# Kernel tuning notes

Hardware: AMD Instinct MI355X
Metric: run time of the kernel (lower is better)

Reference implementation:

```python
import jax, jax.numpy as jnp
from jax import lax
import numpy as np

SEQ = 1024
VOCAB = 50000
EMB = 300
CAS_V, CAS_D = 8, 50
POS_V, POS_D = 48, 50
IN_DIM = EMB + CAS_D + POS_D  # 400
H = 512
T = 13  # num_classes / CRF tags


def setup_inputs() -> dict:
    key = jax.random.key(0)
    ks = jax.random.split(key, 16)
    s = lambda k, shape, sc=0.05: jax.random.normal(k, shape, dtype=jnp.float32) * sc
    return {
        "x": jax.random.randint(ks[0], (SEQ,), 0, VOCAB),
        "casing": jax.random.randint(ks[1], (SEQ,), 0, CAS_V),
        "pos": jax.random.randint(ks[2], (SEQ,), 0, POS_V),
        "h0": jnp.zeros((2, H), dtype=jnp.float32),
        "c0": jnp.zeros((2, H), dtype=jnp.float32),
        "W_emb": s(ks[3], (VOCAB, EMB)),
        "W_cas": s(ks[4], (CAS_V, CAS_D)),
        "W_pos": s(ks[5], (POS_V, POS_D)),
        "Wx_f": s(ks[6], (IN_DIM, 4 * H)),
        "Wh_f": s(ks[7], (H, 4 * H)),
        "b_f": jnp.zeros((4 * H,), dtype=jnp.float32),
        "Wx_b": s(ks[8], (IN_DIM, 4 * H)),
        "Wh_b": s(ks[9], (H, 4 * H)),
        "b_b": jnp.zeros((4 * H,), dtype=jnp.float32),
        "W_out": s(ks[10], (2 * H, T)),
        "b_out": jnp.zeros((T,), dtype=jnp.float32),
        "trans": s(ks[11], (T, T), 0.1),
        "start_trans": s(ks[12], (T,), 0.1),
        "end_trans": s(ks[13], (T,), 0.1),
    }


def _lstm_dir(feat, Wx, Wh, b, h0, c0, reverse):
    # feat: [L, IN_DIM]; precompute input projection for all steps
    pre = feat @ Wx + b  # [L, 4H]

    def step(carry, p):
        h, c = carry
        z = p + h @ Wh
        i, f, g, o = jnp.split(z, 4, axis=-1)
        c = jax.nn.sigmoid(f) * c + jax.nn.sigmoid(i) * jnp.tanh(g)
        h = jax.nn.sigmoid(o) * jnp.tanh(c)
        return (h, c), h

    _, hs = lax.scan(step, (h0, c0), pre, reverse=reverse)
    return hs  # [L, H]


def _viterbi(em, trans, start_trans, end_trans):
    # em: [L, T] emission (log) scores; max-plus DP
    score0 = start_trans + em[0]

    def fwd(score, e):
        total = score[:, None] + trans  # [T, T]: prev -> next
        best = jnp.max(total, axis=0) + e
        idx = jnp.argmax(total, axis=0)
        return best, idx

    final, hist = lax.scan(fwd, score0, em[1:])  # hist: [L-1, T]
    final = final + end_trans
    last = jnp.argmax(final)

    def back(tag, idx_row):
        return idx_row[tag], tag

    first, rest = lax.scan(back, last, hist, reverse=True)
    return jnp.concatenate([first[None], rest])  # [L] int


def reference(x, casing, pos, h0, c0, W_emb, W_cas, W_pos, Wx_f, Wh_f, b_f,
              Wx_b, Wh_b, b_b, W_out, b_out, trans, start_trans, end_trans):
    # AWD-LSTM encode (eval mode: dropout identity)
    feat = jnp.concatenate([W_emb[x], W_cas[casing], W_pos[pos]], axis=-1)  # [L, 400]
    hf = _lstm_dir(feat, Wx_f, Wh_f, b_f, h0[0], c0[0], reverse=False)
    hb = _lstm_dir(feat, Wx_b, Wh_b, b_b, h0[1], c0[1], reverse=True)
    o = jnp.concatenate([hf, hb], axis=-1) @ W_out + b_out  # [L, T]
    tag_scores = jax.nn.log_softmax(o, axis=1)
    path = _viterbi(tag_scores, trans, start_trans, end_trans)
    return tag_scores, path
```

## Files before the change

kernel.cpp:

```cpp
#include <hip/hip_runtime.h>
#include <hip/hip_bf16.h>
#include <math.h>

#define SEQ 1024
#define HID 512
#define FOURH 2048
#define IND 400
#define NT 13

#define NWG_DIR 32
#define LSTM_THREADS 512
#define JPW 16
#define WCOLS 64
#define TAG_INVALID 0xFFFFFFFFu

__device__ __forceinline__ float bf2f(unsigned short u) {
    union { unsigned u32; float f; } v;
    v.u32 = ((unsigned)u) << 16;
    return v.f;
}

__device__ __forceinline__ unsigned short f2bf(float f) {
    union { float f; unsigned u; } v;
    v.f = f;
    unsigned u = v.u;
    unsigned rounding = 0x7FFFu + ((u >> 16) & 1u);
    u += rounding;
    return (unsigned short)(u >> 16);
}

__device__ __forceinline__ float ldf(const void* p, size_t i, int isf32) {
    return isf32 ? ((const float*)p)[i] : bf2f(((const unsigned short*)p)[i]);
}

__device__ __forceinline__ float fsigm(float x) {
    return __builtin_amdgcn_rcpf(1.f + __builtin_amdgcn_exp2f(-1.44269504f * x));
}
__device__ __forceinline__ float ftanhf(float x) {
    return 1.f - 2.f * __builtin_amdgcn_rcpf(__builtin_amdgcn_exp2f(2.88539008f * x) + 1.f);
}
__device__ __forceinline__ float satz(float z) { return fminf(fmaxf(z, -60.f), 60.f); }

__global__ __launch_bounds__(64) void detect_kernel(const unsigned short* __restrict__ w,
                                                    int* __restrict__ flag,
                                                    unsigned* __restrict__ vcnt) {
    int lane = threadIdx.x;
    int cnt = 0;
    for (int i = 0; i < 4; ++i) {
        unsigned short u = w[2 * (lane * 4 + i)];
        int e = (u >> 7) & 0xFF;
        if (e >= 90 && e < 127) cnt++;
    }
#pragma unroll
    for (int off = 32; off >= 1; off >>= 1) cnt += __shfl_xor(cnt, off, 64);
    if (lane == 0) *flag = (cnt < 128) ? 1 : 0;
    if (lane == 1) *vcnt = 0;
}

__global__ __launch_bounds__(256) void pre_gemm_kernel(
        const int* __restrict__ x, const int* __restrict__ cas, const int* __restrict__ pos,
        const void* __restrict__ W_emb, const void* __restrict__ W_cas, const void* __restrict__ W_pos,
        const void* __restrict__ Wx_f, const void* __restrict__ b_f,
        const void* __restrict__ Wx_b, const void* __restrict__ b_b,
        unsigned short* __restrict__ pre, const int* __restrict__ dflag) {
    __shared__ float ftile[32 * IND];
    __shared__ int idxs[96];
    const int isf32 = *dflag;
    int dir = blockIdx.z;
    const void* Wx = dir ? Wx_b : Wx_f;
    const void* bb = dir ? b_b : b_f;
    unsigned short* pre_d = pre + (size_t)dir * SEQ * FOURH;
    int r0 = blockIdx.y * 32;
    int col = blockIdx.x * 256 + threadIdx.x;
    int tid = threadIdx.x;

    if (tid < 32)       idxs[tid] = x[r0 + tid];
    else if (tid < 64)  idxs[tid] = cas[r0 + tid - 32];
    else if (tid < 96)  idxs[tid] = pos[r0 + tid - 64];
    __syncthreads();

    for (int idx = tid; idx < 32 * IND; idx += 256) {
        int r = idx / IND;
        int e = idx - r * IND;
        float v;
        if (e < 300)      v = ldf(W_emb, (size_t)idxs[r] * 300 + e, isf32);
        else if (e < 350) v = ldf(W_cas, (size_t)idxs[32 + r] * 50 + (e - 300), isf32);
        else              v = ldf(W_pos, (size_t)idxs[64 + r] * 50 + (e - 350), isf32);
        ftile[idx] = v;
    }
    __syncthreads();

    float acc[32];
    float bias = ldf(bb, col, isf32);
#pragma unroll
    for (int r = 0; r < 32; ++r) acc[r] = bias;

    if (isf32) {
        const float* W = (const float*)Wx;
        for (int kk = 0; kk < 100; ++kk) {
            int k = kk * 4;
            float w0 = W[(size_t)(k + 0) * FOURH + col];
            float w1 = W[(size_t)(k + 1) * FOURH + col];
            float w2 = W[(size_t)(k + 2) * FOURH + col];
            float w3 = W[(size_t)(k + 3) * FOURH + col];
#pragma unroll
            for (int r = 0; r < 32; ++r) {
                float4 f = *(const float4*)&ftile[r * IND + k];
                acc[r] += f.x * w0 + f.y * w1 + f.z * w2 + f.w * w3;
            }
        }
    } else {
        const unsigned short* W = (const unsigned short*)Wx;
        for (int kk = 0; kk < 100; ++kk) {
            int k = kk * 4;
            float w0 = bf2f(W[(size_t)(k + 0) * FOURH + col]);
            float w1 = bf2f(W[(size_t)(k + 1) * FOURH + col]);
            float w2 = bf2f(W[(size_t)(k + 2) * FOURH + col]);
            float w3 = bf2f(W[(size_t)(k + 3) * FOURH + col]);
#pragma unroll
            for (int r = 0; r < 32; ++r) {
                float4 f = *(const float4*)&ftile[r * IND + k];
                acc[r] += f.x * w0 + f.y * w1 + f.z * w2 + f.w * w3;
            }
        }
    }
    for (int r = 0; r < 32; ++r) pre_d[(size_t)(r0 + r) * FOURH + col] = f2bf(acc[r]);
}

__global__ __launch_bounds__(LSTM_THREADS, 2) void lstm_kernel(
        const void* __restrict__ Wh_f, const void* __restrict__ Wh_b,
        const void* __restrict__ h0, const void* __restrict__ c0,
        const unsigned short* __restrict__ pre, float* __restrict__ hsout,
        unsigned long long* hbuf, const int* __restrict__ dflag) {
    __shared__ float hs[HID];
    __shared__ float red[8 * WCOLS];

    const int isf32 = *dflag;
    const int tid = threadIdx.x;
    const int b = blockIdx.x;
    const int dir = b & 1;
    const int g = b >> 1;
    const int j0 = g * JPW;

    const void* Wh = dir ? Wh_b : Wh_f;
    const unsigned short* pre_d = pre + (size_t)dir * SEQ * FOURH;
    float* hso = hsout + (size_t)dir * SEQ * HID;
    unsigned long long* hb_d = hbuf + dir * 2 * HID;

    const int seg  = tid >> 6;
    const int col  = tid & 63;
    const int unit = col & 15;
    const int gate = col >> 4;
    const int gcol = gate * HID + j0 + unit;
    const int redoff = seg * WCOLS + unit * 4 + gate;

    float wreg[64];
    if (isf32) {
        const float* wp = (const float*)Wh + (size_t)(seg * 64) * FOURH + gcol;
#pragma unroll
        for (int kk = 0; kk < 64; ++kk) wreg[kk] = wp[(size_t)kk * FOURH];
    } else {
        const unsigned short* wp = (const unsigned short*)Wh + (size_t)(seg * 64) * FOURH + gcol;
#pragma unroll
        for (int kk = 0; kk < 64; ++kk) wreg[kk] = bf2f(wp[(size_t)kk * FOURH]);
    }

    float creg = 0.f;
    unsigned short zn0 = 0, zn1 = 0, zn2 = 0, zn3 = 0;
    if (tid < JPW) {
        creg = ldf(c0, dir * HID + j0 + tid, isf32);
        float h0v = ldf(h0, dir * HID + j0 + tid, isf32);
        __hip_atomic_store(&hb_d[j0 + tid],
                           (unsigned long long)__float_as_uint(h0v),
                           __ATOMIC_RELAXED, __HIP_MEMORY_SCOPE_AGENT);
        __hip_atomic_store(&hb_d[HID + j0 + tid],
                           ((unsigned long long)TAG_INVALID << 32),
                           __ATOMIC_RELAXED, __HIP_MEMORY_SCOPE_AGENT);
        int t0 = dir ? (SEQ - 1) : 0;
        zn0 = pre_d[(size_t)t0 * FOURH + 0 * HID + j0 + tid];
        zn1 = pre_d[(size_t)t0 * FOURH + 1 * HID + j0 + tid];
        zn2 = pre_d[(size_t)t0 * FOURH + 2 * HID + j0 + tid];
        zn3 = pre_d[(size_t)t0 * FOURH + 3 * HID + j0 + tid];
    }
    __syncthreads();

    for (int s = 0; s < SEQ; ++s) {
        const int t = dir ? (SEQ - 1 - s) : s;

        {
            const unsigned long long* wp = &hb_d[(s & 1) * HID + tid];
            const unsigned expect = (unsigned)s;
            unsigned long long w;
            do {
                w = __hip_atomic_load(wp, __ATOMIC_RELAXED, __HIP_MEMORY_SCOPE_AGENT);
            } while ((unsigned)(w >> 32) != expect);
            hs[tid] = __uint_as_float((unsigned)w);
        }

        float zc0 = 0.f, zc1 = 0.f, zc2 = 0.f, zc3 = 0.f;
        if (tid < JPW) {
            zc0 = bf2f(zn0); zc1 = bf2f(zn1); zc2 = bf2f(zn2); zc3 = bf2f(zn3);
            if (s + 1 < SEQ) {
                int tn = dir ? (SEQ - 2 - s) : (s + 1);
                zn0 = pre_d[(size_t)tn * FOURH + 0 * HID + j0 + tid];
                zn1 = pre_d[(size_t)tn * FOURH + 1 * HID + j0 + tid];
                zn2 = pre_d[(size_t)tn * FOURH + 2 * HID + j0 + tid];
                zn3 = pre_d[(size_t)tn * FOURH + 3 * HID + j0 + tid];
            }
        }
        __syncthreads();

        float a0 = 0.f, a1 = 0.f, a2 = 0.f, a3 = 0.f;
        const float4* hp = (const float4*)(hs + seg * 64);
#pragma unroll
        for (int q = 0; q < 16; ++q) {
            float4 h4 = hp[q];
            int base = q * 4;
            if ((q & 3) == 0) a0 += h4.x * wreg[base] + h4.y * wreg[base + 1] + h4.z * wreg[base + 2] + h4.w * wreg[base + 3];
            if ((q & 3) == 1) a1 += h4.x * wreg[base] + h4.y * wreg[base + 1] + h4.z * wreg[base + 2] + h4.w * wreg[base + 3];
            if ((q & 3) == 2) a2 += h4.x * wreg[base] + h4.y * wreg[base + 1] + h4.z * wreg[base + 2] + h4.w * wreg[base + 3];
            if ((q & 3) == 3) a3 += h4.x * wreg[base] + h4.y * wreg[base + 1] + h4.z * wreg[base + 2] + h4.w * wreg[base + 3];
        }
        red[redoff] = (a0 + a1) + (a2 + a3);
        __syncthreads();

        if (tid < JPW) {
            int jj = tid;
            float z0 = zc0, z1 = zc1, z2 = zc2, z3 = zc3;
#pragma unroll
            for (int s8 = 0; s8 < 8; ++s8) {
                float4 r4 = *(const float4*)&red[s8 * WCOLS + jj * 4];
                z0 += r4.x; z1 += r4.y; z2 += r4.z; z3 += r4.w;
            }
            z0 = satz(z0); z1 = satz(z1); z2 = satz(z2); z3 = satz(z3);
            float ig = fsigm(z0);
            float fg = fsigm(z1);
            float gg = ftanhf(z2);
            float og = fsigm(z3);
            float cnew = fg * creg + ig * gg;
            creg = cnew;
            float hnew = og * ftanhf(satz(cnew));
            unsigned long long w = ((unsigned long long)(unsigned)(s + 1) << 32)
                                 | (unsigned long long)__float_as_uint(hnew);
            __hip_atomic_store(&hb_d[((s + 1) & 1) * HID + j0 + jj], w,
                               __ATOMIC_RELAXED, __HIP_MEMORY_SCOPE_AGENT);
            hso[(size_t)t * HID + j0 + jj] = hnew;
        }
    }
}

__global__ __launch_bounds__(64) void outproj_kernel(const float* __restrict__ hsout,
        const void* __restrict__ W_out, const void* __restrict__ b_out,
        float* __restrict__ out_scores,
        const void* __restrict__ trans, const void* __restrict__ strans,
        const void* __restrict__ etrans, float* __restrict__ out_path,
        unsigned* __restrict__ vcnt, const int* __restrict__ dflag) {
    __shared__ unsigned char hist[SEQ][NT];
    const int isf32 = *dflag;
    int t = blockIdx.x;
    int lane = threadIdx.x;
    const float* hf = hsout + (size_t)t * HID;
    const float* hb = hsout + (size_t)SEQ * HID + (size_t)t * HID;
    float acc[NT];
#pragma unroll
    for (int j = 0; j < NT; ++j) acc[j] = 0.f;
    for (int k = lane; k < HID; k += 64) {
        float a = hf[k], b2 = hb[k];
#pragma unroll
        for (int j = 0; j < NT; ++j)
            acc[j] += a * ldf(W_out, (size_t)k * NT + j, isf32)
                    + b2 * ldf(W_out, (size_t)(HID + k) * NT + j, isf32);
    }
#pragma unroll
    for (int off = 32; off >= 1; off >>= 1) {
#pragma unroll
        for (int j = 0; j < NT; ++j) acc[j] += __shfl_xor(acc[j], off, 64);
    }
    float o[NT];
    float m = -1e30f;
#pragma unroll
    for (int j = 0; j < NT; ++j) { o[j] = acc[j] + ldf(b_out, j, isf32); m = fmaxf(m, o[j]); }
    float lse = 0.f;
#pragma unroll
    for (int j = 0; j < NT; ++j) lse += expf(o[j] - m);
    lse = m + logf(lse);
    if (lane < NT)
        __hip_atomic_store(&out_scores[t * NT + lane], o[lane] - lse,
                           __ATOMIC_RELAXED, __HIP_MEMORY_SCOPE_AGENT);
    __builtin_amdgcn_s_waitcnt(0);

    unsigned old = 0;
    if (lane == 0) old = atomicAdd(vcnt, 1u);
    old = __shfl(old, 0, 64);
    if (old != SEQ - 1) return;

    const float* em = out_scores;
    int j = lane < NT ? lane : 0;
    float tr[NT];
#pragma unroll
    for (int i = 0; i < NT; ++i) tr[i] = ldf(trans, i * NT + j, isf32);
    float score = ldf(strans, j, isf32)
                + __hip_atomic_load(&em[j], __ATOMIC_RELAXED, __HIP_MEMORY_SCOPE_AGENT);
    float pe_next = __hip_atomic_load(&em[NT + j], __ATOMIC_RELAXED, __HIP_MEMORY_SCOPE_AGENT);
    for (int tt = 1; tt < SEQ; ++tt) {
        float pe = pe_next;
        if (tt + 1 < SEQ)
            pe_next = __hip_atomic_load(&em[(tt + 1) * NT + j],
                                        __ATOMIC_RELAXED, __HIP_MEMORY_SCOPE_AGENT);
        float best = -1e30f;
        int arg = 0;
#pragma unroll
        for (int i = 0; i < NT; ++i) {
            float si = __shfl(score, i, 64);
            float cand = si + tr[i];
            if (cand > best) { best = cand; arg = i; }
        }
        if (lane < NT) hist[tt][lane] = (unsigned char)arg;
        score = best + pe;
    }
    score += ldf(etrans, j, isf32);
    float bmax = -1e30f;
    int last = 0;
#pragma unroll
    for (int i = 0; i < NT; ++i) {
        float si = __shfl(score, i, 64);
        if (si > bmax) { bmax = si; last = i; }
    }
    if (lane == 0) {
        int cur = last;
        out_path[SEQ - 1] = (float)cur;
        for (int tt = SEQ - 1; tt >= 1; --tt) {
            cur = hist[tt][cur];
            out_path[tt - 1] = (float)cur;
        }
    }
}

extern "C" void kernel_launch(void* const* d_in, const int* in_sizes, int n_in,
                              void* d_out, int out_size, void* d_ws, size_t ws_size,
                              hipStream_t stream) {
    const int* x      = (const int*)d_in[0];
    const int* casing = (const int*)d_in[1];
    const int* posi   = (const int*)d_in[2];
    const void* h0    = d_in[3];
    const void* c0    = d_in[4];
    const void* W_emb = d_in[5];
    const void* W_cas = d_in[6];
    const void* W_pos = d_in[7];
    const void* Wx_f  = d_in[8];
    const void* Wh_f  = d_in[9];
    const void* b_f   = d_in[10];
    const void* Wx_b  = d_in[11];
    const void* Wh_b  = d_in[12];
    const void* b_b   = d_in[13];
    const void* W_out = d_in[14];
    const void* b_out = d_in[15];
    const void* trans = d_in[16];
    const void* strans = d_in[17];
    const void* etrans = d_in[18];

    char* ws = (char*)d_ws;
    int* dflag          = (int*)(ws + 448);
    unsigned* vcnt      = (unsigned*)(ws + 456);
    unsigned short* pre = (unsigned short*)(ws + 512);
    float* hsout        = (float*)(ws + 512 + 8388608);
    unsigned long long* hbuf = (unsigned long long*)(ws + 512 + 8388608 + 4194304);

    float* out_scores = (float*)d_out;
    float* out_path   = out_scores + SEQ * NT;

    detect_kernel<<<1, 64, 0, stream>>>((const unsigned short*)W_emb, dflag, vcnt);

    dim3 g2(8, 32, 2);
    pre_gemm_kernel<<<g2, 256, 0, stream>>>(x, casing, posi, W_emb, W_cas, W_pos,
                                            Wx_f, b_f, Wx_b, b_b, pre, dflag);

    lstm_kernel<<<2 * NWG_DIR, LSTM_THREADS, 0, stream>>>(
        Wh_f, Wh_b, h0, c0, pre, hsout, hbuf, dflag);

    outproj_kernel<<<SEQ, 64, 0, stream>>>(hsout, W_out, b_out, out_scores,
                                           trans, strans, etrans, out_path, vcnt, dflag);
}
```

Baseline: 2.520 ms.

## Broadcast hidden state via readlane, drop a barrier, batch Viterbi emission prefetch

```diff
diff --git a/kernel.cpp b/kernel.cpp
--- a/kernel.cpp
+++ b/kernel.cpp
@@ -132,8 +132,7 @@
         const void* __restrict__ h0, const void* __restrict__ c0,
         const unsigned short* __restrict__ pre, float* __restrict__ hsout,
         unsigned long long* hbuf, const int* __restrict__ dflag) {
-    __shared__ float hs[HID];
-    __shared__ float red[8 * WCOLS];
+    __shared__ float red[2][8 * WCOLS];
 
     const int isf32 = *dflag;
     const int tid = threadIdx.x;
@@ -154,15 +153,21 @@
     const int gcol = gate * HID + j0 + unit;
     const int redoff = seg * WCOLS + unit * 4 + gate;
 
-    float wreg[64];
+    float4 w0, w1, w2, w3, w4, w5, w6, w7, w8, w9, w10, w11, w12, w13, w14, w15;
     if (isf32) {
         const float* wp = (const float*)Wh + (size_t)(seg * 64) * FOURH + gcol;
-#pragma unroll
-        for (int kk = 0; kk < 64; ++kk) wreg[kk] = wp[(size_t)kk * FOURH];
+#define LDW(i) w##i = make_float4(wp[(size_t)(4*i+0)*FOURH], wp[(size_t)(4*i+1)*FOURH], \
+                                  wp[(size_t)(4*i+2)*FOURH], wp[(size_t)(4*i+3)*FOURH])
+        LDW(0); LDW(1); LDW(2); LDW(3); LDW(4); LDW(5); LDW(6); LDW(7);
+        LDW(8); LDW(9); LDW(10); LDW(11); LDW(12); LDW(13); LDW(14); LDW(15);
+#undef LDW
     } else {
         const unsigned short* wp = (const unsigned short*)Wh + (size_t)(seg * 64) * FOURH + gcol;
-#pragma unroll
-        for (int kk = 0; kk < 64; ++kk) wreg[kk] = bf2f(wp[(size_t)kk * FOURH]);
+#define LDW(i) w##i = make_float4(bf2f(wp[(size_t)(4*i+0)*FOURH]), bf2f(wp[(size_t)(4*i+1)*FOURH]), \
+                                  bf2f(wp[(size_t)(4*i+2)*FOURH]), bf2f(wp[(size_t)(4*i+3)*FOURH]))
+        LDW(0); LDW(1); LDW(2); LDW(3); LDW(4); LDW(5); LDW(6); LDW(7);
+        LDW(8); LDW(9); LDW(10); LDW(11); LDW(12); LDW(13); LDW(14); LDW(15);
+#undef LDW
     }
 
     float creg = 0.f;
@@ -187,6 +192,7 @@
     for (int s = 0; s < SEQ; ++s) {
         const int t = dir ? (SEQ - 1 - s) : s;
 
+        unsigned hu;
         {
             const unsigned long long* wp = &hb_d[(s & 1) * HID + tid];
             const unsigned expect = (unsigned)s;
@@ -194,7 +200,7 @@
             do {
                 w = __hip_atomic_load(wp, __ATOMIC_RELAXED, __HIP_MEMORY_SCOPE_AGENT);
             } while ((unsigned)(w >> 32) != expect);
-            hs[tid] = __uint_as_float((unsigned)w);
+            hu = (unsigned)w;
         }
 
         float zc0 = 0.f, zc1 = 0.f, zc2 = 0.f, zc3 = 0.f;
@@ -208,28 +214,29 @@
                 zn3 = pre_d[(size_t)tn * FOURH + 3 * HID + j0 + tid];
             }
         }
-        __syncthreads();
 
         float a0 = 0.f, a1 = 0.f, a2 = 0.f, a3 = 0.f;
-        const float4* hp = (const float4*)(hs + seg * 64);
-#pragma unroll
-        for (int q = 0; q < 16; ++q) {
-            float4 h4 = hp[q];
-            int base = q * 4;
-            if ((q & 3) == 0) a0 += h4.x * wreg[base] + h4.y * wreg[base + 1] + h4.z * wreg[base + 2] + h4.w * wreg[base + 3];
-            if ((q & 3) == 1) a1 += h4.x * wreg[base] + h4.y * wreg[base + 1] + h4.z * wreg[base + 2] + h4.w * wreg[base + 3];
-            if ((q & 3) == 2) a2 += h4.x * wreg[base] + h4.y * wreg[base + 1] + h4.z * wreg[base + 2] + h4.w * wreg[base + 3];
-            if ((q & 3) == 3) a3 += h4.x * wreg[base] + h4.y * wreg[base + 1] + h4.z * wreg[base + 2] + h4.w * wreg[base + 3];
-        }
-        red[redoff] = (a0 + a1) + (a2 + a3);
+#define MACQ(i, A) { \
+        float hx = __uint_as_float((unsigned)__builtin_amdgcn_readlane((int)hu, 4*i+0)); \
+        float hy = __uint_as_float((unsigned)__builtin_amdgcn_readlane((int)hu, 4*i+1)); \
+        float hz = __uint_as_float((unsigned)__builtin_amdgcn_readlane((int)hu, 4*i+2)); \
+        float hw = __uint_as_float((unsigned)__builtin_amdgcn_readlane((int)hu, 4*i+3)); \
+        A += hx * w##i.x + hy * w##i.y + hz * w##i.z + hw * w##i.w; }
+        MACQ(0, a0)  MACQ(1, a1)  MACQ(2, a2)  MACQ(3, a3)
+        MACQ(4, a0)  MACQ(5, a1)  MACQ(6, a2)  MACQ(7, a3)
+        MACQ(8, a0)  MACQ(9, a1)  MACQ(10, a2) MACQ(11, a3)
+        MACQ(12, a0) MACQ(13, a1) MACQ(14, a2) MACQ(15, a3)
+#undef MACQ
+        red[s & 1][redoff] = (a0 + a1) + (a2 + a3);
         __syncthreads();
 
         if (tid < JPW) {
             int jj = tid;
             float z0 = zc0, z1 = zc1, z2 = zc2, z3 = zc3;
+            const float* rp = &red[s & 1][0];
 #pragma unroll
             for (int s8 = 0; s8 < 8; ++s8) {
-                float4 r4 = *(const float4*)&red[s8 * WCOLS + jj * 4];
+                float4 r4 = *(const float4*)&rp[s8 * WCOLS + jj * 4];
                 z0 += r4.x; z1 += r4.y; z2 += r4.z; z3 += r4.w;
             }
             z0 = satz(z0); z1 = satz(z1); z2 = satz(z2); z3 = satz(z3);
@@ -299,25 +306,43 @@
     float tr[NT];
 #pragma unroll
     for (int i = 0; i < NT; ++i) tr[i] = ldf(trans, i * NT + j, isf32);
-    float score = ldf(strans, j, isf32)
-                + __hip_atomic_load(&em[j], __ATOMIC_RELAXED, __HIP_MEMORY_SCOPE_AGENT);
-    float pe_next = __hip_atomic_load(&em[NT + j], __ATOMIC_RELAXED, __HIP_MEMORY_SCOPE_AGENT);
-    for (int tt = 1; tt < SEQ; ++tt) {
-        float pe = pe_next;
-        if (tt + 1 < SEQ)
-            pe_next = __hip_atomic_load(&em[(tt + 1) * NT + j],
-                                        __ATOMIC_RELAXED, __HIP_MEMORY_SCOPE_AGENT);
-        float best = -1e30f;
-        int arg = 0;
-#pragma unroll
-        for (int i = 0; i < NT; ++i) {
-            float si = __shfl(score, i, 64);
-            float cand = si + tr[i];
-            if (cand > best) { best = cand; arg = i; }
-        }
-        if (lane < NT) hist[tt][lane] = (unsigned char)arg;
-        score = best + pe;
-    }
+#define EML(tt) __hip_atomic_load(&em[(size_t)(tt) * NT + j], __ATOMIC_RELAXED, __HIP_MEMORY_SCOPE_AGENT)
+    float score = ldf(strans, j, isf32) + EML(0);
+    float c0 = EML(1), c1 = EML(2), c2 = EML(3), c3 = EML(4),
+          c4 = EML(5), c5 = EML(6), c6 = EML(7), c7 = EML(8);
+#define VSTEP(PE, TT) { \
+    float best = -1e30f; int arg = 0; \
+    _Pragma("unroll") \
+    for (int i = 0; i < NT; ++i) { \
+        float si = __shfl(score, i, 64); \
+        float cand = si + tr[i]; \
+        if (cand > best) { best = cand; arg = i; } \
+    } \
+    if (lane < NT) hist[TT][lane] = (unsigned char)arg; \
+    score = best + PE; }
+    for (int tb = 1; tb < SEQ; tb += 8) {
+        int nb = tb + 8;
+        float n0 = 0.f, n1 = 0.f, n2 = 0.f, n3 = 0.f, n4 = 0.f, n5 = 0.f, n6 = 0.f, n7 = 0.f;
+        if (nb + 0 < SEQ) n0 = EML(nb + 0);
+        if (nb + 1 < SEQ) n1 = EML(nb + 1);
+        if (nb + 2 < SEQ) n2 = EML(nb + 2);
+        if (nb + 3 < SEQ) n3 = EML(nb + 3);
+        if (nb + 4 < SEQ) n4 = EML(nb + 4);
+        if (nb + 5 < SEQ) n5 = EML(nb + 5);
+        if (nb + 6 < SEQ) n6 = EML(nb + 6);
+        if (nb + 7 < SEQ) n7 = EML(nb + 7);
+        VSTEP(c0, tb + 0)
+        if (tb + 1 < SEQ) VSTEP(c1, tb + 1)
+        if (tb + 2 < SEQ) VSTEP(c2, tb + 2)
+        if (tb + 3 < SEQ) VSTEP(c3, tb + 3)
+        if (tb + 4 < SEQ) VSTEP(c4, tb + 4)
+        if (tb + 5 < SEQ) VSTEP(c5, tb + 5)
+        if (tb + 6 < SEQ) VSTEP(c6, tb + 6)
+        if (tb + 7 < SEQ) VSTEP(c7, tb + 7)
+        c0 = n0; c1 = n1; c2 = n2; c3 = n3; c4 = n4; c5 = n5; c6 = n6; c7 = n7;
+    }
+#undef VSTEP
+#undef EML
     score += ldf(etrans, j, isf32);
     float bmax = -1e30f;
     int last = 0;
```

New measurement: 2.301 ms. -8.7%, faster.
